# Kernel optimization log

Hardware: AMD Instinct MI355X
Metric: run time of the kernel (lower is better)

## Reference

```python
import jax, jax.numpy as jnp
import numpy as np

N_NODE, N_GRAPH, EMBED_DIM, NUM_HEADS = 512, 16, 768, 12
HEAD_DIM = EMBED_DIM // NUM_HEADS


def setup_inputs() -> dict:
    key = jax.random.key(0)
    ks = jax.random.split(key, 12)
    s = 1.0 / np.sqrt(EMBED_DIM)
    inp = {
        "x": jax.random.normal(ks[0], (N_NODE, N_GRAPH, EMBED_DIM), jnp.float32),
        "attn_bias": jax.random.normal(ks[1], (N_GRAPH, NUM_HEADS, N_NODE, N_NODE), jnp.float32),
        "attn_mask": jnp.zeros((N_NODE, N_NODE), jnp.float32),
        "key_padding_mask": jnp.zeros((N_GRAPH, N_NODE), dtype=bool),
        "wq": jax.random.normal(ks[2], (EMBED_DIM, EMBED_DIM), jnp.float32) * s,
        "bq": jax.random.normal(ks[3], (EMBED_DIM,), jnp.float32) * 0.01,
        "wk": jax.random.normal(ks[4], (EMBED_DIM, EMBED_DIM), jnp.float32) * s,
        "bk": jax.random.normal(ks[5], (EMBED_DIM,), jnp.float32) * 0.01,
        "wv": jax.random.normal(ks[6], (EMBED_DIM, EMBED_DIM), jnp.float32) * s,
        "bv": jax.random.normal(ks[7], (EMBED_DIM,), jnp.float32) * 0.01,
        "wo": jax.random.normal(ks[8], (EMBED_DIM, EMBED_DIM), jnp.float32) * s,
        "bo": jax.random.normal(ks[9], (EMBED_DIM,), jnp.float32) * 0.01,
    }
    return inp


def reference(x, attn_bias, attn_mask, key_padding_mask, wq, bq, wk, bk, wv, bv, wo, bo):
    n_node, n_graph, embed_dim = x.shape
    h, d = NUM_HEADS, HEAD_DIM
    scaling = d ** (-0.5)
    # projections (eqx Linear: x @ W.T + b)
    q = (x @ wq.T + bq) * scaling
    k = x @ wk.T + bk
    v = x @ wv.T + bv
    # (n_node, n_graph*h, d) -> (n_graph*h, n_node, d)
    q = q.reshape(n_node, n_graph * h, d).transpose((1, 0, 2))
    k = k.reshape(n_node, n_graph * h, d).transpose((1, 0, 2))
    v = v.reshape(n_node, n_graph * h, d).transpose((1, 0, 2))
    # (n_graph*h, n_node, n_node)
    attn_weights = jnp.einsum("bqd,bkd->bqk", q, k)
    attn_weights = attn_weights + attn_bias.reshape(n_graph * h, n_node, n_node)
    attn_weights = attn_weights + attn_mask[None, :, :]
    # key padding mask: (n_graph, n_node) -> broadcast over heads and query dim
    pad = key_padding_mask[:, None, None, :]  # (n_graph, 1, 1, n_node)
    attn_weights = attn_weights.reshape(n_graph, h, n_node, n_node)
    attn_weights = jnp.where(pad, float("-inf"), attn_weights)
    attn_weights = attn_weights.reshape(n_graph * h, n_node, n_node)
    attn_probs = jax.nn.softmax(attn_weights.astype(jnp.float32), axis=-1)
    attn = jnp.einsum("bqk,bkd->bqd", attn_probs, v)
    attn = attn.transpose((1, 0, 2)).reshape(n_node, n_graph, embed_dim)
    return attn @ wo.T + bo
```

## Files before the change

kernel.cpp:

```cpp
#include <hip/hip_runtime.h>
#include <cstdint>
#include <cstddef>

#define N_NODE 512
#define N_GRAPH 16
#define EMBED 768
#define NHEAD 12
#define HDIM 64
#define NB (N_GRAPH * NHEAD)
#define MROWS (N_NODE * N_GRAPH)

typedef __attribute__((ext_vector_type(8))) __bf16 bf16x8;
typedef __attribute__((ext_vector_type(4))) float f32x4;
typedef __attribute__((ext_vector_type(4))) unsigned short u16x4;

__device__ inline unsigned short f2bf(float f) {
  unsigned u = __builtin_bit_cast(unsigned, f);
  u += 0x7fff + ((u >> 16) & 1);
  return (unsigned short)(u >> 16);
}

__device__ inline void gload_lds16(const void* g, void* l) {
  __builtin_amdgcn_global_load_lds(
      (const __attribute__((address_space(1))) void*)g,
      (__attribute__((address_space(3))) void*)l, 16, 0, 0);
}

__global__ void cvt_kernel(const float* __restrict__ in,
                           unsigned short* __restrict__ out, int n4) {
  int i = blockIdx.x * blockDim.x + threadIdx.x;
  if (i >= n4) return;
  f32x4 v = reinterpret_cast<const f32x4*>(in)[i];
  u16x4 o;
  o.x = f2bf(v.x); o.y = f2bf(v.y); o.z = f2bf(v.z); o.w = f2bf(v.w);
  reinterpret_cast<u16x4*>(out)[i] = o;
}

__global__ __launch_bounds__(256) void qkv_gemm(
    const unsigned short* __restrict__ xb,
    const unsigned short* __restrict__ wqb, const unsigned short* __restrict__ wkb,
    const unsigned short* __restrict__ wvb,
    const float* __restrict__ bq, const float* __restrict__ bk,
    const float* __restrict__ bv,
    unsigned short* __restrict__ qo, unsigned short* __restrict__ ko,
    unsigned short* __restrict__ vto) {
  __shared__ unsigned short As[128 * 32];
  __shared__ unsigned short Bs[128 * 32];
  const int z = blockIdx.z;
  const unsigned short* W = (z == 0) ? wqb : (z == 1) ? wkb : wvb;
  const float* bias = (z == 0) ? bq : (z == 1) ? bk : bv;
  const int m0 = blockIdx.x * 128, n0 = blockIdx.y * 128;
  const int tid = threadIdx.x;
  const int w = tid >> 6, lane = tid & 63, g = lane >> 4, c = lane & 15;
  const int wm = (w >> 1) * 64, wn = (w & 1) * 64;
  const int t1 = w * 128 + lane, t2 = t1 + 64;
  const unsigned short* a1 = xb + (size_t)(m0 + (t1 >> 2)) * EMBED + (t1 & 3) * 8;
  const unsigned short* a2 = xb + (size_t)(m0 + (t2 >> 2)) * EMBED + (t2 & 3) * 8;
  const unsigned short* b1 = W + (size_t)(n0 + (t1 >> 2)) * EMBED + (t1 & 3) * 8;
  const unsigned short* b2 = W + (size_t)(n0 + (t2 >> 2)) * EMBED + (t2 & 3) * 8;
  char* asb = (char*)As + w * 2048;
  char* bsb = (char*)Bs + w * 2048;
  f32x4 acc[4][4] = {};
  for (int k0 = 0; k0 < EMBED; k0 += 32) {
    gload_lds16(a1 + k0, asb);
    gload_lds16(a2 + k0, asb + 1024);
    gload_lds16(b1 + k0, bsb);
    gload_lds16(b2 + k0, bsb + 1024);
    __syncthreads();
    bf16x8 af[4], bfr[4];
#pragma unroll
    for (int mi = 0; mi < 4; ++mi)
      af[mi] = *reinterpret_cast<const bf16x8*>(&As[(wm + mi * 16 + c) * 32 + g * 8]);
#pragma unroll
    for (int ni = 0; ni < 4; ++ni)
      bfr[ni] = *reinterpret_cast<const bf16x8*>(&Bs[(wn + ni * 16 + c) * 32 + g * 8]);
#pragma unroll
    for (int mi = 0; mi < 4; ++mi)
#pragma unroll
      for (int ni = 0; ni < 4; ++ni)
        acc[mi][ni] = __builtin_amdgcn_mfma_f32_16x16x32_bf16(af[mi], bfr[ni],
                                                              acc[mi][ni], 0, 0, 0);
    __syncthreads();
  }
#pragma unroll
  for (int mi = 0; mi < 4; ++mi) {
#pragma unroll
    for (int ni = 0; ni < 4; ++ni) {
#pragma unroll
      for (int i = 0; i < 4; ++i) {
        int m = m0 + wm + mi * 16 + g * 4 + i;
        int n = n0 + wn + ni * 16 + c;
        float v = acc[mi][ni][i] + bias[n];
        int node = m >> 4, graph = m & 15, head = n >> 6, d = n & 63;
        size_t bidx = (size_t)(graph * NHEAD + head);
        if (z == 0) {
          v *= 0.125f;
          qo[(bidx * N_NODE + node) * HDIM + d] = f2bf(v);
        } else if (z == 1) {
          ko[(bidx * N_NODE + node) * HDIM + d] = f2bf(v);
        } else {
          vto[(bidx * HDIM + d) * N_NODE + node] = f2bf(v);
        }
      }
    }
  }
}

__global__ __launch_bounds__(256) void attn_kernel(
    const unsigned short* __restrict__ qb, const unsigned short* __restrict__ kb,
    const unsigned short* __restrict__ vtb, const float* __restrict__ bias,
    const float* __restrict__ amask, const unsigned char* __restrict__ kpm,
    unsigned short* __restrict__ attn_out) {
  __shared__ unsigned short P[4][16 * 72];
  const int b = blockIdx.y, qt = blockIdx.x;
  const int tid = threadIdx.x;
  const int w = tid >> 6, lane = tid & 63, g = lane >> 4, c = lane & 15;
  const int graph = b / NHEAD, head = b % NHEAD;
  const int qbase = qt * 64 + w * 16;
  const size_t bQ = (size_t)b * N_NODE;
  const unsigned short* qptr = qb + (bQ + qbase + c) * HDIM + g * 8;
  bf16x8 aq0 = *reinterpret_cast<const bf16x8*>(qptr);
  bf16x8 aq1 = *reinterpret_cast<const bf16x8*>(qptr + 32);
  f32x4 o[4] = {};
  float m_run[4], l_run[4];
#pragma unroll
  for (int i = 0; i < 4; ++i) { m_run[i] = -INFINITY; l_run[i] = 0.0f; }
  unsigned short* Pw = P[w];
  for (int it = 0; it < 8; ++it) {
    const int kbk = it * 64;
    f32x4 s[4];
#pragma unroll
    for (int kf = 0; kf < 4; ++kf) {
      const unsigned short* kp = kb + (bQ + kbk + kf * 16 + c) * HDIM + g * 8;
      bf16x8 b0 = *reinterpret_cast<const bf16x8*>(kp);
      bf16x8 b1 = *reinterpret_cast<const bf16x8*>(kp + 32);
      f32x4 acc = {};
      acc = __builtin_amdgcn_mfma_f32_16x16x32_bf16(aq0, b0, acc, 0, 0, 0);
      acc = __builtin_amdgcn_mfma_f32_16x16x32_bf16(aq1, b1, acc, 0, 0, 0);
      s[kf] = acc;
    }
#pragma unroll
    for (int kf = 0; kf < 4; ++kf) {
      const int key = kbk + kf * 16 + c;
      const unsigned char pm = kpm[graph * N_NODE + key];
#pragma unroll
      for (int i = 0; i < 4; ++i) {
        const int q = qbase + g * 4 + i;
        float v;
        if (pm) {
          v = -1e30f;
        } else {
          v = s[kf][i] + bias[((size_t)b * N_NODE + q) * N_NODE + key] +
              amask[(size_t)q * N_NODE + key];
        }
        s[kf][i] = v;
      }
    }
    float mx[4];
#pragma unroll
    for (int i = 0; i < 4; ++i)
      mx[i] = fmaxf(fmaxf(s[0][i], s[1][i]), fmaxf(s[2][i], s[3][i]));
#pragma unroll
    for (int xm = 1; xm < 16; xm <<= 1)
#pragma unroll
      for (int i = 0; i < 4; ++i) mx[i] = fmaxf(mx[i], __shfl_xor(mx[i], xm, 64));
    float rs[4];
#pragma unroll
    for (int i = 0; i < 4; ++i) {
      float mn = fmaxf(m_run[i], mx[i]);
      float sc = __expf(m_run[i] - mn);
      m_run[i] = mn;
      l_run[i] *= sc;
      o[0][i] *= sc; o[1][i] *= sc; o[2][i] *= sc; o[3][i] *= sc;
      rs[i] = 0.0f;
    }
#pragma unroll
    for (int kf = 0; kf < 4; ++kf)
#pragma unroll
      for (int i = 0; i < 4; ++i) {
        float p = __expf(s[kf][i] - m_run[i]);
        rs[i] += p;
        Pw[(g * 4 + i) * 72 + kf * 16 + c] = f2bf(p);
      }
#pragma unroll
    for (int xm = 1; xm < 16; xm <<= 1)
#pragma unroll
      for (int i = 0; i < 4; ++i) rs[i] += __shfl_xor(rs[i], xm, 64);
#pragma unroll
    for (int i = 0; i < 4; ++i) l_run[i] += rs[i];
    asm volatile("s_waitcnt lgkmcnt(0)" ::: "memory");
#pragma unroll
    for (int kc = 0; kc < 2; ++kc) {
      bf16x8 ap = *reinterpret_cast<const bf16x8*>(&Pw[c * 72 + kc * 32 + g * 8]);
#pragma unroll
      for (int dt = 0; dt < 4; ++dt) {
        const unsigned short* vp =
            vtb + ((size_t)b * HDIM + dt * 16 + c) * N_NODE + kbk + kc * 32 + g * 8;
        bf16x8 bv = *reinterpret_cast<const bf16x8*>(vp);
        o[dt] = __builtin_amdgcn_mfma_f32_16x16x32_bf16(ap, bv, o[dt], 0, 0, 0);
      }
    }
  }
#pragma unroll
  for (int i = 0; i < 4; ++i) {
    float inv = 1.0f / l_run[i];
    int node = qbase + g * 4 + i;
#pragma unroll
    for (int dt = 0; dt < 4; ++dt) {
      int d = dt * 16 + c;
      attn_out[((size_t)(node * N_GRAPH + graph)) * EMBED + head * HDIM + d] =
          f2bf(o[dt][i] * inv);
    }
  }
}

__global__ __launch_bounds__(256) void oproj_gemm(
    const unsigned short* __restrict__ ab, const unsigned short* __restrict__ wob,
    const float* __restrict__ bo, float* __restrict__ out) {
  __shared__ unsigned short As[128 * 32];
  __shared__ unsigned short Bs[128 * 32];
  const int m0 = blockIdx.x * 128, n0 = blockIdx.y * 128;
  const int tid = threadIdx.x;
  const int w = tid >> 6, lane = tid & 63, g = lane >> 4, c = lane & 15;
  const int wm = (w >> 1) * 64, wn = (w & 1) * 64;
  const int t1 = w * 128 + lane, t2 = t1 + 64;
  const unsigned short* a1 = ab + (size_t)(m0 + (t1 >> 2)) * EMBED + (t1 & 3) * 8;
  const unsigned short* a2 = ab + (size_t)(m0 + (t2 >> 2)) * EMBED + (t2 & 3) * 8;
  const unsigned short* b1 = wob + (size_t)(n0 + (t1 >> 2)) * EMBED + (t1 & 3) * 8;
  const unsigned short* b2 = wob + (size_t)(n0 + (t2 >> 2)) * EMBED + (t2 & 3) * 8;
  char* asb = (char*)As + w * 2048;
  char* bsb = (char*)Bs + w * 2048;
  f32x4 acc[4][4] = {};
  for (int k0 = 0; k0 < EMBED; k0 += 32) {
    gload_lds16(a1 + k0, asb);
    gload_lds16(a2 + k0, asb + 1024);
    gload_lds16(b1 + k0, bsb);
    gload_lds16(b2 + k0, bsb + 1024);
    __syncthreads();
    bf16x8 af[4], bfr[4];
#pragma unroll
    for (int mi = 0; mi < 4; ++mi)
      af[mi] = *reinterpret_cast<const bf16x8*>(&As[(wm + mi * 16 + c) * 32 + g * 8]);
#pragma unroll
    for (int ni = 0; ni < 4; ++ni)
      bfr[ni] = *reinterpret_cast<const bf16x8*>(&Bs[(wn + ni * 16 + c) * 32 + g * 8]);
#pragma unroll
    for (int mi = 0; mi < 4; ++mi)
#pragma unroll
      for (int ni = 0; ni < 4; ++ni)
        acc[mi][ni] = __builtin_amdgcn_mfma_f32_16x16x32_bf16(af[mi], bfr[ni],
                                                              acc[mi][ni], 0, 0, 0);
    __syncthreads();
  }
#pragma unroll
  for (int mi = 0; mi < 4; ++mi) {
#pragma unroll
    for (int ni = 0; ni < 4; ++ni) {
#pragma unroll
      for (int i = 0; i < 4; ++i) {
        int m = m0 + wm + mi * 16 + g * 4 + i;
        int n = n0 + wn + ni * 16 + c;
        out[(size_t)m * EMBED + n] = acc[mi][ni][i] + bo[n];
      }
    }
  }
}

extern "C" void kernel_launch(void* const* d_in, const int* in_sizes, int n_in,
                              void* d_out, int out_size, void* d_ws, size_t ws_size,
                              hipStream_t stream) {
  const float* x = (const float*)d_in[0];
  const float* attn_bias = (const float*)d_in[1];
  const float* attn_mask = (const float*)d_in[2];
  const unsigned char* kpm = (const unsigned char*)d_in[3];
  const float* wq = (const float*)d_in[4];
  const float* bq = (const float*)d_in[5];
  const float* wk = (const float*)d_in[6];
  const float* bk = (const float*)d_in[7];
  const float* wv = (const float*)d_in[8];
  const float* bv = (const float*)d_in[9];
  const float* wo = (const float*)d_in[10];
  const float* bo = (const float*)d_in[11];

  char* ws = (char*)d_ws;
  const size_t xbf_b = (size_t)MROWS * EMBED * 2;
  const size_t wbf_b = (size_t)EMBED * EMBED * 2;
  const size_t qkv_b = (size_t)NB * N_NODE * HDIM * 2;
  unsigned short* x_bf = (unsigned short*)ws;  ws += xbf_b;
  unsigned short* wq_bf = (unsigned short*)ws; ws += wbf_b;
  unsigned short* wk_bf = (unsigned short*)ws; ws += wbf_b;
  unsigned short* wv_bf = (unsigned short*)ws; ws += wbf_b;
  unsigned short* wo_bf = (unsigned short*)ws; ws += wbf_b;
  unsigned short* q_bf = (unsigned short*)ws;  ws += qkv_b;
  unsigned short* k_bf = (unsigned short*)ws;  ws += qkv_b;
  unsigned short* vt_bf = (unsigned short*)ws; ws += qkv_b;
  unsigned short* attn_bf = (unsigned short*)ws;

  const int n4x = MROWS * EMBED / 4;
  const int n4w = EMBED * EMBED / 4;
  cvt_kernel<<<(n4x + 255) / 256, 256, 0, stream>>>(x, x_bf, n4x);
  cvt_kernel<<<(n4w + 255) / 256, 256, 0, stream>>>(wq, wq_bf, n4w);
  cvt_kernel<<<(n4w + 255) / 256, 256, 0, stream>>>(wk, wk_bf, n4w);
  cvt_kernel<<<(n4w + 255) / 256, 256, 0, stream>>>(wv, wv_bf, n4w);
  cvt_kernel<<<(n4w + 255) / 256, 256, 0, stream>>>(wo, wo_bf, n4w);

  qkv_gemm<<<dim3(MROWS / 128, EMBED / 128, 3), 256, 0, stream>>>(
      x_bf, wq_bf, wk_bf, wv_bf, bq, bk, bv, q_bf, k_bf, vt_bf);

  attn_kernel<<<dim3(N_NODE / 64, NB), 256, 0, stream>>>(
      q_bf, k_bf, vt_bf, attn_bias, attn_mask, kpm, attn_bf);

  oproj_gemm<<<dim3(MROWS / 128, EMBED / 128), 256, 0, stream>>>(
      attn_bf, wo_bf, bo, (float*)d_out);
}
```

Baseline: 589.0 us.

## Transpose QK^T MFMA so each lane owns a query row with vectorized bias loads

```diff
diff --git a/kernel.cpp b/kernel.cpp
--- a/kernel.cpp
+++ b/kernel.cpp
@@ -122,9 +122,10 @@
   bf16x8 aq0 = *reinterpret_cast<const bf16x8*>(qptr);
   bf16x8 aq1 = *reinterpret_cast<const bf16x8*>(qptr + 32);
   f32x4 o[4] = {};
-  float m_run[4], l_run[4];
-#pragma unroll
-  for (int i = 0; i < 4; ++i) { m_run[i] = -INFINITY; l_run[i] = 0.0f; }
+  float m_run = -INFINITY, l_run = 0.0f;
+  const float* bias_row = bias + ((size_t)b * N_NODE + qbase + c) * N_NODE;
+  const float* amask_row = amask + (size_t)(qbase + c) * N_NODE;
+  const unsigned char* kpm_row = kpm + graph * N_NODE;
   unsigned short* Pw = P[w];
   for (int it = 0; it < 8; ++it) {
     const int kbk = it * 64;
@@ -135,59 +136,54 @@
       bf16x8 b0 = *reinterpret_cast<const bf16x8*>(kp);
       bf16x8 b1 = *reinterpret_cast<const bf16x8*>(kp + 32);
       f32x4 acc = {};
-      acc = __builtin_amdgcn_mfma_f32_16x16x32_bf16(aq0, b0, acc, 0, 0, 0);
-      acc = __builtin_amdgcn_mfma_f32_16x16x32_bf16(aq1, b1, acc, 0, 0, 0);
+      acc = __builtin_amdgcn_mfma_f32_16x16x32_bf16(b0, aq0, acc, 0, 0, 0);
+      acc = __builtin_amdgcn_mfma_f32_16x16x32_bf16(b1, aq1, acc, 0, 0, 0);
       s[kf] = acc;
     }
 #pragma unroll
     for (int kf = 0; kf < 4; ++kf) {
-      const int key = kbk + kf * 16 + c;
-      const unsigned char pm = kpm[graph * N_NODE + key];
+      const int k4 = kbk + kf * 16 + g * 4;
+      f32x4 bv4 = *reinterpret_cast<const f32x4*>(bias_row + k4);
+      f32x4 mv4 = *reinterpret_cast<const f32x4*>(amask_row + k4);
+      unsigned pm4 = *reinterpret_cast<const unsigned*>(kpm_row + k4);
 #pragma unroll
       for (int i = 0; i < 4; ++i) {
-        const int q = qbase + g * 4 + i;
-        float v;
-        if (pm) {
-          v = -1e30f;
-        } else {
-          v = s[kf][i] + bias[((size_t)b * N_NODE + q) * N_NODE + key] +
-              amask[(size_t)q * N_NODE + key];
-        }
-        s[kf][i] = v;
-      }
-    }
-    float mx[4];
-#pragma unroll
-    for (int i = 0; i < 4; ++i)
-      mx[i] = fmaxf(fmaxf(s[0][i], s[1][i]), fmaxf(s[2][i], s[3][i]));
-#pragma unroll
-    for (int xm = 1; xm < 16; xm <<= 1)
-#pragma unroll
-      for (int i = 0; i < 4; ++i) mx[i] = fmaxf(mx[i], __shfl_xor(mx[i], xm, 64));
-    float rs[4];
-#pragma unroll
-    for (int i = 0; i < 4; ++i) {
-      float mn = fmaxf(m_run[i], mx[i]);
-      float sc = __expf(m_run[i] - mn);
-      m_run[i] = mn;
-      l_run[i] *= sc;
-      o[0][i] *= sc; o[1][i] *= sc; o[2][i] *= sc; o[3][i] *= sc;
-      rs[i] = 0.0f;
-    }
+        float v = s[kf][i] + bv4[i] + mv4[i];
+        s[kf][i] = ((pm4 >> (8 * i)) & 0xffu) ? -1e30f : v;
+      }
+    }
+    float mx = s[0][0];
 #pragma unroll
     for (int kf = 0; kf < 4; ++kf)
 #pragma unroll
+      for (int i = 0; i < 4; ++i) mx = fmaxf(mx, s[kf][i]);
+    mx = fmaxf(mx, __shfl_xor(mx, 16, 64));
+    mx = fmaxf(mx, __shfl_xor(mx, 32, 64));
+    const float mn = fmaxf(m_run, mx);
+    const float sc = __expf(m_run - mn);
+    m_run = mn;
+    float rs = 0.0f;
+#pragma unroll
+    for (int kf = 0; kf < 4; ++kf) {
+      u16x4 pw;
+#pragma unroll
       for (int i = 0; i < 4; ++i) {
-        float p = __expf(s[kf][i] - m_run[i]);
-        rs[i] += p;
-        Pw[(g * 4 + i) * 72 + kf * 16 + c] = f2bf(p);
-      }
-#pragma unroll
-    for (int xm = 1; xm < 16; xm <<= 1)
-#pragma unroll
-      for (int i = 0; i < 4; ++i) rs[i] += __shfl_xor(rs[i], xm, 64);
-#pragma unroll
-    for (int i = 0; i < 4; ++i) l_run[i] += rs[i];
+        float p = __expf(s[kf][i] - mn);
+        rs += p;
+        pw[i] = f2bf(p);
+      }
+      *reinterpret_cast<u16x4*>(&Pw[c * 72 + kf * 16 + g * 4]) = pw;
+    }
+    rs += __shfl_xor(rs, 16, 64);
+    rs += __shfl_xor(rs, 32, 64);
+    l_run = l_run * sc + rs;
+    float scq[4];
+#pragma unroll
+    for (int i = 0; i < 4; ++i) scq[i] = __shfl(sc, (lane >> 4) * 4 + i, 64);
+#pragma unroll
+    for (int dt = 0; dt < 4; ++dt)
+#pragma unroll
+      for (int i = 0; i < 4; ++i) o[dt][i] *= scq[i];
     asm volatile("s_waitcnt lgkmcnt(0)" ::: "memory");
 #pragma unroll
     for (int kc = 0; kc < 2; ++kc) {
@@ -201,15 +197,18 @@
       }
     }
   }
+  float invq[4];
+#pragma unroll
+  for (int i = 0; i < 4; ++i)
+    invq[i] = 1.0f / __shfl(l_run, (lane >> 4) * 4 + i, 64);
 #pragma unroll
   for (int i = 0; i < 4; ++i) {
-    float inv = 1.0f / l_run[i];
     int node = qbase + g * 4 + i;
 #pragma unroll
     for (int dt = 0; dt < 4; ++dt) {
       int d = dt * 16 + c;
       attn_out[((size_t)(node * N_GRAPH + graph)) * EMBED + head * HDIM + d] =
-          f2bf(o[dt][i] * inv);
+          f2bf(o[dt][i] * invq[i]);
     }
   }
 }
```

New measurement: 536.1 us. 1.1x faster.
